# Kernel tuning notes

Measured on AMD Instinct MI355X. Metric: run time of the kernel, lower is better.

Reference implementation:

```python
import jax, jax.numpy as jnp
import numpy as np

N_WIRES = 4
# Fixed realization of tq.RandomLayer(n_ops=8, wires=[0..3]):
# a deterministic sequence of 8 parameterized gates with angles theta[k].
RANDOM_OPS = [
    ("rx", (0,)), ("ry", (1,)), ("rz", (3,)), ("crx", (0, 2)),
    ("ry", (3,)), ("rx", (2,)), ("crx", (1, 3)), ("rz", (0,)),
]


def _ry(t):
    c = jnp.cos(t / 2).astype(jnp.complex64)
    s = jnp.sin(t / 2).astype(jnp.complex64)
    return jnp.stack([jnp.stack([c, -s]), jnp.stack([s, c])])


def _rx(t):
    c = jnp.cos(t / 2).astype(jnp.complex64)
    s = jnp.sin(t / 2).astype(jnp.complex64)
    return jnp.stack([jnp.stack([c, -1j * s]), jnp.stack([-1j * s, c])])


def _rz(t):
    e0 = jnp.exp(-1j * (t / 2)).astype(jnp.complex64)
    e1 = jnp.exp(1j * (t / 2)).astype(jnp.complex64)
    z = jnp.zeros((), jnp.complex64)
    return jnp.stack([jnp.stack([e0, z]), jnp.stack([z, e1])])


def _crx(t):
    U = _rx(t)
    z2 = jnp.zeros((2, 2), jnp.complex64)
    i2 = jnp.eye(2, dtype=jnp.complex64)
    return jnp.concatenate([jnp.concatenate([i2, z2], 1), jnp.concatenate([z2, U], 1)], 0)


def _apply_1q(psi, U, w):
    # psi: (N,2,2,2,2); apply 2x2 gate on wire w
    psi = jnp.moveaxis(psi, 1 + w, -1)
    psi = psi @ U.T
    return jnp.moveaxis(psi, -1, 1 + w)


def _apply_2q(psi, U4, w1, w2):
    psi = jnp.moveaxis(psi, (1 + w1, 1 + w2), (-2, -1))
    shp = psi.shape
    psi = (psi.reshape(shp[:-2] + (4,)) @ U4.T).reshape(shp)
    return jnp.moveaxis(psi, (-2, -1), (1 + w1, 1 + w2))


def _quanv_forward(x, theta, W, b):
    B = x.shape[0]
    img = x.reshape(B, 28, 28)
    # 2x2 stride-2 patches, order [x[r,c], x[r,c+1], x[r+1,c], x[r+1,c+1]]
    patches = img.reshape(B, 14, 2, 14, 2).transpose(0, 1, 3, 2, 4).reshape(B * 196, 4)
    # RY-encoded product state: ry(a)|0> = [cos(a/2), sin(a/2)]
    half = patches * 0.5
    c = jnp.cos(half).astype(jnp.complex64)
    s = jnp.sin(half).astype(jnp.complex64)
    v = jnp.stack([c, s], axis=-1)  # (N, 4 wires, 2)
    psi = jnp.einsum('na,nb,nc,nd->nabcd', v[:, 0], v[:, 1], v[:, 2], v[:, 3])
    gate_fns = {"rx": _rx, "ry": _ry, "rz": _rz}
    for k, (name, wires) in enumerate(RANDOM_OPS):
        t = theta[k]
        if name == "crx":
            psi = _apply_2q(psi, _crx(t), wires[0], wires[1])
        else:
            psi = _apply_1q(psi, gate_fns[name](t), wires[0])
    probs = (psi.real ** 2 + psi.imag ** 2).reshape(-1, 16)  # (N,16)
    # PauliZ expectation per wire; wire 0 is the most significant bit
    idx = jnp.arange(16)
    bits = (idx[:, None] >> (3 - jnp.arange(N_WIRES)[None, :])) & 1
    z_table = (1.0 - 2.0 * bits).astype(jnp.float32)  # (16,4)
    meas = probs @ z_table  # (N,4)
    feats = meas.reshape(B, 196 * 4)  # (B,784), patch-major like torch.cat
    logits = feats @ W.T + b
    return jax.nn.log_softmax(logits, axis=-1)


def setup_inputs() -> dict:
    key = jax.random.key(0)
    k1, k2, k3 = jax.random.split(key, 3)
    B = 2048
    x = jax.random.normal(k1, (B, 1, 28, 28), jnp.float32)
    theta = jax.random.normal(k2, (8,), jnp.float32)
    W = jax.random.normal(k3, (10, 784), jnp.float32) * 0.02
    b = jnp.zeros((10,), jnp.float32)
    return {"x": x, "theta": theta, "W": W, "b": b}


def reference(x, theta, W, b):
    return _quanv_forward(x, theta, W, b)
```

## Files before the change

kernel.cpp:

```cpp
#include <hip/hip_runtime.h>
#include <math.h>


__device__ __forceinline__ float wave_sum_dpp(float v) {
#define DPP_ADD(CTRL, RMASK)                                                  \
    v += __int_as_float(__builtin_amdgcn_update_dpp(                          \
        0, __float_as_int(v), (CTRL), (RMASK), 0xf, true))
    DPP_ADD(0x111, 0xf);
    DPP_ADD(0x112, 0xf);
    DPP_ADD(0x114, 0xf);
    DPP_ADD(0x118, 0xf);
    DPP_ADD(0x142, 0xa);
    DPP_ADD(0x143, 0xc);
#undef DPP_ADD
    return __int_as_float(__builtin_amdgcn_readlane(__float_as_int(v), 63));
}

__global__ __launch_bounds__(256) void quanv_fused_kernel(
    const float* __restrict__ xin,
    const float* __restrict__ theta,
    const float* __restrict__ Wm,
    const float* __restrict__ bv,
    float* __restrict__ out,
    int B)
{
    const int t = threadIdx.x;
    const int w = t >> 6, l = t & 63;
    const int img = blockIdx.x * 4 + w;
    if (img >= B) return;

    const float* ib = xin + (size_t)img * 784;
    const bool tail = (l < 4);

    float2 rA[4], rB[4];
#pragma unroll
    for (int k = 0; k < 3; ++k) {
        const int p = l + 64 * k;
        const int pi = p / 14, pj = p % 14;
        const float* pr = ib + pi * 56 + pj * 2;
        rA[k] = *(const float2*)pr;
        rB[k] = *(const float2*)(pr + 28);
    }
    if (tail) {
        const int p = 192 + l;
        const int pi = p / 14, pj = p % 14;
        const float* pr = ib + pi * 56 + pj * 2;
        rA[3] = *(const float2*)pr;
        rB[3] = *(const float2*)(pr + 28);
    }

    const float t0 = theta[0], th1 = theta[1], t2 = theta[2], t3 = theta[3];
    const float t4 = theta[4], t5 = theta[5], t6 = theta[6];
    const float c5g = __cosf(t5), c35 = __cosf(t3 + t5);
    const float c6 = __cosf(t6), s6 = __sinf(t6);
    const float k0 = __cosf(t0);
    const float A  = 0.5f * (c5g + c35);
    const float Bc = 0.5f * k0 * (c5g - c35);
    const float C1 = 0.5f * (1.f + c6);
    const float C2 = 0.5f * (1.f - c6);
    const float K1 = __cosf(t4);
    const float K2 = -__sinf(t4) * __cosf(t2);
    const float C5 = 0.5f * s6 * __sinf(t2);

    auto featf = [&](float2 a, float2 b) -> float4 {
        const float ca0 = __cosf(a.x);
        const float u   = __cosf(a.y + th1);
        const float ca2 = __cosf(b.x);
        float sa3, ca3;
        __sincosf(b.y, &sa3, &ca3);
        const float m0 = k0 * ca0;
        const float m2 = ca2 * fmaf(Bc, ca0, A);
        const float zu = fmaf(K1, ca3, K2 * sa3);
        const float m3 = fmaf(fmaf(C2, u, C1), zu, C5 * sa3 * (1.f - u));
        return make_float4(m0, u, m2, m3);
    };

    float acc[10];
#pragma unroll
    for (int c = 0; c < 10; ++c) acc[c] = 0.f;

    const float4* W4 = (const float4*)Wm;
#pragma unroll
    for (int k = 0; k < 3; ++k) {
        const float4 f = featf(rA[k], rB[k]);
        const int p = l + 64 * k;
#pragma unroll
        for (int c = 0; c < 10; ++c) {
            const float4 wv = W4[c * 196 + p];
            acc[c] = fmaf(f.w, wv.w, fmaf(f.z, wv.z,
                     fmaf(f.y, wv.y, fmaf(f.x, wv.x, acc[c]))));
        }
    }
    if (tail) {
        const float4 f = featf(rA[3], rB[3]);
        const int p = 192 + l;
#pragma unroll
        for (int c = 0; c < 10; ++c) {
            const float4 wv = W4[c * 196 + p];
            acc[c] = fmaf(f.w, wv.w, fmaf(f.z, wv.z,
                     fmaf(f.y, wv.y, fmaf(f.x, wv.x, acc[c]))));
        }
    }

    float logit[10];
#pragma unroll
    for (int c = 0; c < 10; ++c) logit[c] = wave_sum_dpp(acc[c]) + bv[c];

    float mx = -1e30f;
#pragma unroll
    for (int c = 0; c < 10; ++c) mx = fmaxf(mx, logit[c]);
    float sum = 0.f;
#pragma unroll
    for (int c = 0; c < 10; ++c) sum += __expf(logit[c] - mx);
    const float ls = __logf(sum);

    if (l < 10) {
        float v = logit[9];
#pragma unroll
        for (int c = 8; c >= 0; --c) v = (l == c) ? logit[c] : v;
        out[(size_t)img * 10 + l] = v - mx - ls;
    }
}

extern "C" void kernel_launch(void* const* d_in, const int* in_sizes, int n_in,
                              void* d_out, int out_size, void* d_ws, size_t ws_size,
                              hipStream_t stream) {
    const float* x     = (const float*)d_in[0];
    const float* theta = (const float*)d_in[1];
    const float* W     = (const float*)d_in[2];
    const float* bias  = (const float*)d_in[3];
    float* out         = (float*)d_out;

    const int B = in_sizes[0] / 784;
    const int grid = (B + 3) / 4;
    quanv_fused_kernel<<<grid, 256, 0, stream>>>(x, theta, W, bias, out, B);
}
```

Baseline: 10.47 us.

## Split each image's patches across two waves and combine partials via LDS

Each image is now handled by two wavefronts, each covering 98 patches, where before one wave handled all 196. The two partial logit vectors are combined through shared memory before log-softmax. The intent is to double the number of waves in flight and shorten the per-wave serial chain of loads and FMAs, which improves latency hiding. In exchange it adds a block barrier, LDS traffic, a second DPP reduction per image, and idle lanes in the second patch pass.

Result: no change. 10.53 us (+0.6%).

```diff
diff --git a/kernel.cpp b/kernel.cpp
--- a/kernel.cpp
+++ b/kernel.cpp
@@ -16,7 +16,7 @@
     return __int_as_float(__builtin_amdgcn_readlane(__float_as_int(v), 63));
 }
 
-__global__ __launch_bounds__(256) void quanv_fused_kernel(
+__global__ __launch_bounds__(512) void quanv_fused_kernel(
     const float* __restrict__ xin,
     const float* __restrict__ theta,
     const float* __restrict__ Wm,
@@ -24,29 +24,31 @@
     float* __restrict__ out,
     int B)
 {
+    __shared__ float part[8][10];
+
     const int t = threadIdx.x;
     const int w = t >> 6, l = t & 63;
-    const int img = blockIdx.x * 4 + w;
-    if (img >= B) return;
+    const int imgRaw = blockIdx.x * 4 + (w >> 1);
+    const int img = (imgRaw < B) ? imgRaw : (B - 1);
+    const int h = w & 1;
 
     const float* ib = xin + (size_t)img * 784;
-    const bool tail = (l < 4);
+    const int p0 = h * 98 + l;
+    const bool two = (l < 34);
+    const int p1 = p0 + 64;
 
-    float2 rA[4], rB[4];
-#pragma unroll
-    for (int k = 0; k < 3; ++k) {
-        const int p = l + 64 * k;
-        const int pi = p / 14, pj = p % 14;
+    float2 rA0, rB0, rA1, rB1;
+    {
+        const int pi = p0 / 14, pj = p0 % 14;
         const float* pr = ib + pi * 56 + pj * 2;
-        rA[k] = *(const float2*)pr;
-        rB[k] = *(const float2*)(pr + 28);
+        rA0 = *(const float2*)pr;
+        rB0 = *(const float2*)(pr + 28);
     }
-    if (tail) {
-        const int p = 192 + l;
-        const int pi = p / 14, pj = p % 14;
+    if (two) {
+        const int pi = p1 / 14, pj = p1 % 14;
         const float* pr = ib + pi * 56 + pj * 2;
-        rA[3] = *(const float2*)pr;
-        rB[3] = *(const float2*)(pr + 28);
+        rA1 = *(const float2*)pr;
+        rB1 = *(const float2*)(pr + 28);
     }
 
     const float t0 = theta[0], th1 = theta[1], t2 = theta[2], t3 = theta[3];
@@ -80,45 +82,57 @@
     for (int c = 0; c < 10; ++c) acc[c] = 0.f;
 
     const float4* W4 = (const float4*)Wm;
-#pragma unroll
-    for (int k = 0; k < 3; ++k) {
-        const float4 f = featf(rA[k], rB[k]);
-        const int p = l + 64 * k;
+    {
+        const float4 f = featf(rA0, rB0);
 #pragma unroll
         for (int c = 0; c < 10; ++c) {
-            const float4 wv = W4[c * 196 + p];
+            const float4 wv = W4[c * 196 + p0];
             acc[c] = fmaf(f.w, wv.w, fmaf(f.z, wv.z,
                      fmaf(f.y, wv.y, fmaf(f.x, wv.x, acc[c]))));
         }
     }
-    if (tail) {
-        const float4 f = featf(rA[3], rB[3]);
-        const int p = 192 + l;
+    if (two) {
+        const float4 f = featf(rA1, rB1);
 #pragma unroll
         for (int c = 0; c < 10; ++c) {
-            const float4 wv = W4[c * 196 + p];
+            const float4 wv = W4[c * 196 + p1];
             acc[c] = fmaf(f.w, wv.w, fmaf(f.z, wv.z,
                      fmaf(f.y, wv.y, fmaf(f.x, wv.x, acc[c]))));
         }
     }
 
-    float logit[10];
+    float partial[10];
 #pragma unroll
-    for (int c = 0; c < 10; ++c) logit[c] = wave_sum_dpp(acc[c]) + bv[c];
-
-    float mx = -1e30f;
-#pragma unroll
-    for (int c = 0; c < 10; ++c) mx = fmaxf(mx, logit[c]);
-    float sum = 0.f;
-#pragma unroll
-    for (int c = 0; c < 10; ++c) sum += __expf(logit[c] - mx);
-    const float ls = __logf(sum);
+    for (int c = 0; c < 10; ++c) partial[c] = wave_sum_dpp(acc[c]);
 
     if (l < 10) {
-        float v = logit[9];
+        float v = partial[9];
 #pragma unroll
-        for (int c = 8; c >= 0; --c) v = (l == c) ? logit[c] : v;
-        out[(size_t)img * 10 + l] = v - mx - ls;
+        for (int c = 8; c >= 0; --c) v = (l == c) ? partial[c] : v;
+        part[w][l] = v;
+    }
+    __syncthreads();
+
+    if (h == 0) {
+        float logit[10];
+#pragma unroll
+        for (int c = 0; c < 10; ++c)
+            logit[c] = part[w][c] + part[w + 1][c] + bv[c];
+
+        float mx = -1e30f;
+#pragma unroll
+        for (int c = 0; c < 10; ++c) mx = fmaxf(mx, logit[c]);
+        float sum = 0.f;
+#pragma unroll
+        for (int c = 0; c < 10; ++c) sum += __expf(logit[c] - mx);
+        const float ls = __logf(sum);
+
+        if (l < 10 && imgRaw < B) {
+            float v = logit[9];
+#pragma unroll
+            for (int c = 8; c >= 0; --c) v = (l == c) ? logit[c] : v;
+            out[(size_t)imgRaw * 10 + l] = v - mx - ls;
+        }
     }
 }
 
@@ -133,5 +147,5 @@
 
     const int B = in_sizes[0] / 784;
     const int grid = (B + 3) / 4;
-    quanv_fused_kernel<<<grid, 256, 0, stream>>>(x, theta, W, bias, out, B);
+    quanv_fused_kernel<<<grid, 512, 0, stream>>>(x, theta, W, bias, out, B);
 }
```
